# Optimization experiments

Hardware: AMD Instinct MI355X
Metric: run time of the kernel (lower is better)

Reference implementation:

```python
import jax, jax.numpy as jnp
import numpy as np

D = 512       # hidden_size (attention defaults hardcode 512)
N = 8         # num_heads
H = D // N    # depth per head = 64
FF = 2048     # FFN filter size (hardcoded)
EPS = 1e-6


def _layer_norm(x, gamma, beta):
    # matches functional layer_norm: biased variance, eps inside sqrt
    mean = jnp.mean(x, axis=-1, keepdims=True)
    var = jnp.mean((x - mean) ** 2, axis=-1, keepdims=True)
    return gamma * ((x - mean) / jnp.sqrt(var + EPS)) + beta


def setup_inputs() -> dict:
    key = jax.random.key(0)
    ks = jax.random.split(key, 12)
    B, S = 8, 1024
    s = lambda k, shape, scale: jax.random.normal(k, shape, jnp.float32) * scale
    return {
        "inputs": s(ks[0], (B, S, D), 1.0),
        "attention_bias": jnp.zeros((B, 1, 1, S), jnp.float32),
        "ln1_g": jnp.ones((D,), jnp.float32),
        "ln1_b": jnp.zeros((D,), jnp.float32),
        "wq": s(ks[1], (D, N, H), D ** -0.5),
        "wk": s(ks[2], (D, N, H), D ** -0.5),
        "wv": s(ks[3], (D, N, H), D ** -0.5),
        "wo": s(ks[4], (N, H, D), D ** -0.5),
        "ln2_g": jnp.ones((D,), jnp.float32),
        "ln2_b": jnp.zeros((D,), jnp.float32),
        "w1": s(ks[5], (D, FF), D ** -0.5),
        "b1": jnp.zeros((FF,), jnp.float32),
        "w2": s(ks[6], (FF, D), FF ** -0.5),
        "b2": jnp.zeros((D,), jnp.float32),
    }


def reference(inputs, attention_bias, ln1_g, ln1_b, wq, wk, wv, wo,
              ln2_g, ln2_b, w1, b1, w2, b2):
    # --- self-attention block (pre-LN, residual) ---
    y = _layer_norm(inputs, ln1_g, ln1_b)
    q = jnp.einsum('bsd,dnh->bsnh', y, wq) * (H ** -0.5)
    k = jnp.einsum('bsd,dnh->bsnh', y, wk)
    v = jnp.einsum('bsd,dnh->bsnh', y, wv)
    # logits[b,n,f,t] = sum_h k[b,t,n,h] * q[b,f,n,h]
    logits = jnp.einsum('btnh,bfnh->bnft', k, q) + attention_bias
    weights = jax.nn.softmax(logits, axis=3)
    attn = jnp.einsum('bnft,btnh->bfnh', weights, v)
    attn_out = jnp.einsum('bfnh,nhd->bfd', attn, wo)
    x = inputs + attn_out

    # --- FFN block (pre-LN, residual) ---
    y2 = _layer_norm(x, ln2_g, ln2_b)
    h = jax.nn.relu(jnp.einsum('bsd,df->bsf', y2, w1) + b1)
    ffn_out = jnp.einsum('bsf,fd->bsd', h, w2) + b2
    return x + ffn_out
```

## Files before the change

### kernel.cpp

```cpp
#include <hip/hip_runtime.h>
#include <stdint.h>

typedef unsigned short u16;
typedef __attribute__((ext_vector_type(8))) __bf16 bf16x8;
typedef __attribute__((ext_vector_type(2))) __bf16 bf16x2;
typedef __attribute__((ext_vector_type(4))) float f32x4;

__device__ __forceinline__ float bf2f(u16 u) {
    union { unsigned int i; float f; } c; c.i = ((unsigned int)u) << 16; return c.f;
}
__device__ __forceinline__ u16 f2bf_sw(float f) {
    union { float f; unsigned int i; } c; c.f = f;
    unsigned int u = c.i;
    u += 0x7FFFu + ((u >> 16) & 1u);
    return (u16)(u >> 16);
}
__device__ __forceinline__ unsigned f2bf2(float lo, float hi) {
#if __has_builtin(__builtin_amdgcn_cvt_pk_bf16_f32)
    union { bf16x2 v; unsigned u; } c;
    c.v = __builtin_amdgcn_cvt_pk_bf16_f32(lo, hi);
    return c.u;
#else
    return (unsigned)f2bf_sw(lo) | ((unsigned)f2bf_sw(hi) << 16);
#endif
}
__device__ __forceinline__ u16 f2bf(float f) {
#if __has_builtin(__builtin_amdgcn_cvt_pk_bf16_f32)
    return (u16)(f2bf2(f, 0.f) & 0xFFFFu);
#else
    return f2bf_sw(f);
#endif
}
__device__ __forceinline__ bool sniff_f32(const unsigned* probe) {
    return probe && ((*probe & 0xFFFFu) == 0u);
}
__device__ __forceinline__ float lde(const void* p, size_t i, bool isf32) {
    return isf32 ? ((const float*)p)[i] : bf2f(((const u16*)p)[i]);
}
__device__ __forceinline__ void g2lds16(const void* g, void* l) {
    __builtin_amdgcn_global_load_lds(
        (__attribute__((address_space(1))) void*)(uintptr_t)g,
        (__attribute__((address_space(3))) void*)(unsigned int)(uintptr_t)l,
        16, 0, 0);
}

__global__ void prep_weights(const void* __restrict__ wq, const void* __restrict__ wk,
                             const void* __restrict__ wv, const void* __restrict__ wo,
                             const void* __restrict__ w1, const void* __restrict__ w2,
                             u16* __restrict__ wqkvT, u16* __restrict__ woT,
                             u16* __restrict__ w1T, u16* __restrict__ w2T,
                             const unsigned* probe) {
    __shared__ u16 t[32][33];
    const bool isf32 = sniff_f32(probe);
    const int id = blockIdx.x;
    const void* src; u16* dst; int R, C, cb, rb; float scale = 1.f;
    if (id < 1024) {
        const int which = id >> 8, tl = id & 255;
        R = 512; C = 512; cb = (tl & 15) * 32; rb = (tl >> 4) * 32;
        if (which == 0)      { src = wq; dst = wqkvT;              scale = 0.18033688011112042f; }
        else if (which == 1) { src = wk; dst = wqkvT + 512 * 512; }
        else if (which == 2) { src = wv; dst = wqkvT + 1024 * 512; }
        else                 { src = wo; dst = woT; }
    } else if (id < 2048) {
        const int tl = id - 1024; src = w1; dst = w1T; R = 512; C = 2048;
        cb = (tl & 63) * 32; rb = (tl >> 6) * 32;
    } else {
        const int tl = id - 2048; src = w2; dst = w2T; R = 2048; C = 512;
        cb = (tl & 15) * 32; rb = (tl >> 4) * 32;
    }
    const int tx = threadIdx.x, ty = threadIdx.y;
#pragma unroll
    for (int i = 0; i < 4; i++)
        t[ty + i * 8][tx] = f2bf(lde(src, (size_t)(rb + ty + i * 8) * C + cb + tx, isf32));
    __syncthreads();
#pragma unroll
    for (int i = 0; i < 4; i++) {
        float v = bf2f(t[tx][ty + i * 8]) * scale;
        dst[(size_t)(cb + ty + i * 8) * R + rb + tx] = f2bf(v);
    }
}

__global__ __launch_bounds__(256) void ln_any(const void* __restrict__ x,
                                              const void* __restrict__ gw,
                                              const void* __restrict__ bw,
                                              u16* __restrict__ y,
                                              const unsigned* probe_x,
                                              const unsigned* probe_gb) {
    const bool xf32 = sniff_f32(probe_x);
    const bool gf32 = sniff_f32(probe_gb);
    const int lane = threadIdx.x & 63, wave = threadIdx.x >> 6;
    const int r = blockIdx.x * 4 + wave;
    union U8 { uint4 v; u16 s[8]; };
    float xs[8];
    if (xf32) {
        const float4* xr = (const float4*)((const float*)x + (size_t)r * 512 + lane * 8);
        float4 p0 = xr[0], p1 = xr[1];
        xs[0]=p0.x; xs[1]=p0.y; xs[2]=p0.z; xs[3]=p0.w;
        xs[4]=p1.x; xs[5]=p1.y; xs[6]=p1.z; xs[7]=p1.w;
    } else {
        U8 xu; xu.v = *(const uint4*)((const u16*)x + (size_t)r * 512 + lane * 8);
#pragma unroll
        for (int j = 0; j < 8; j++) xs[j] = bf2f(xu.s[j]);
    }
    float s1 = 0.f, s2 = 0.f;
#pragma unroll
    for (int j = 0; j < 8; j++) { s1 += xs[j]; s2 += xs[j] * xs[j]; }
#pragma unroll
    for (int d = 1; d < 64; d <<= 1) { s1 += __shfl_xor(s1, d); s2 += __shfl_xor(s2, d); }
    const float mean = s1 * (1.f / 512.f);
    const float var = s2 * (1.f / 512.f) - mean * mean;
    const float rstd = rsqrtf(var + 1e-6f);
    float gs[8], bs[8];
    if (gf32) {
        const float4* gr = (const float4*)((const float*)gw + lane * 8);
        const float4* br = (const float4*)((const float*)bw + lane * 8);
        float4 g0 = gr[0], g1 = gr[1], b0 = br[0], b1 = br[1];
        gs[0]=g0.x; gs[1]=g0.y; gs[2]=g0.z; gs[3]=g0.w; gs[4]=g1.x; gs[5]=g1.y; gs[6]=g1.z; gs[7]=g1.w;
        bs[0]=b0.x; bs[1]=b0.y; bs[2]=b0.z; bs[3]=b0.w; bs[4]=b1.x; bs[5]=b1.y; bs[6]=b1.z; bs[7]=b1.w;
    } else {
        U8 gu; gu.v = *(const uint4*)((const u16*)gw + lane * 8);
        U8 bu; bu.v = *(const uint4*)((const u16*)bw + lane * 8);
#pragma unroll
        for (int j = 0; j < 8; j++) { gs[j] = bf2f(gu.s[j]); bs[j] = bf2f(bu.s[j]); }
    }
    uint4 ov;
    float o[8];
#pragma unroll
    for (int j = 0; j < 8; j++) o[j] = gs[j] * ((xs[j] - mean) * rstd) + bs[j];
    ov.x = f2bf2(o[0], o[1]); ov.y = f2bf2(o[2], o[3]);
    ov.z = f2bf2(o[4], o[5]); ov.w = f2bf2(o[6], o[7]);
    *(uint4*)(y + (size_t)r * 512 + lane * 8) = ov;
}

template <int EPI, int TM>
__global__ __launch_bounds__(256, 2) void gemm_bt(const u16* __restrict__ A,
                                                  const u16* __restrict__ Bt,
                                                  const void* __restrict__ bias,
                                                  const void* __restrict__ res,
                                                  void* __restrict__ out,
                                                  u16* __restrict__ out2,
                                                  const unsigned* probe,
                                                  int M, int N, int K) {
    constexpr int ACH = TM / 16;
    constexpr int MI = TM / 32;
    __shared__ __align__(16) u16 lA[2][TM * 32];
    __shared__ __align__(16) u16 lB[2][128 * 32];
    const int tid = threadIdx.x, wave = tid >> 6, lane = tid & 63;
    const int m0 = blockIdx.x * TM, n0 = blockIdx.y * 128;
    const int wm = (wave >> 1) * (TM / 2), wn = (wave & 1) * 64;
    const int row = lane & 15, quad = lane >> 4;
    f32x4 acc[MI][4];
#pragma unroll
    for (int i = 0; i < MI; i++)
#pragma unroll
        for (int j = 0; j < 4; j++) acc[i][j] = (f32x4){0.f, 0.f, 0.f, 0.f};
    const u16* Ab = A + (size_t)m0 * K;
    const u16* Bb = Bt + (size_t)n0 * K;

    auto stage = [&](int buf, int k0) {
#pragma unroll
        for (int c = 0; c < (ACH + 8 + 3) / 4; c++) {
            const int ch = c * 4 + wave;
            if (ch < ACH) {
                const int e = ch * 64 + lane;
                const int r = e >> 2, col = (e & 3) * 8;
                g2lds16(Ab + (size_t)r * K + k0 + col, (char*)lA[buf] + ch * 1024);
            } else if (ch < ACH + 8) {
                const int c2 = ch - ACH;
                const int e = c2 * 64 + lane;
                const int r = e >> 2, col = (e & 3) * 8;
                g2lds16(Bb + (size_t)r * K + k0 + col, (char*)lB[buf] + c2 * 1024);
            }
        }
    };

    stage(0, 0);
    int cur = 0;
    for (int k0 = 0; k0 < K; k0 += 32) {
        __syncthreads();
        if (k0 + 32 < K) stage(cur ^ 1, k0 + 32);
        bf16x8 af[MI], bfr[4];
#pragma unroll
        for (int t = 0; t < MI; t++)
            af[t]  = *(const bf16x8*)(lA[cur] + (wm + t * 16 + row) * 32 + quad * 8);
#pragma unroll
        for (int t = 0; t < 4; t++)
            bfr[t] = *(const bf16x8*)(lB[cur] + (wn + t * 16 + row) * 32 + quad * 8);
#pragma unroll
        for (int i = 0; i < MI; i++)
#pragma unroll
            for (int j = 0; j < 4; j++)
                acc[i][j] = __builtin_amdgcn_mfma_f32_16x16x32_bf16(af[i], bfr[j], acc[i][j], 0, 0, 0);
        cur ^= 1;
    }
    const bool isf32 = sniff_f32(probe);
#pragma unroll
    for (int i = 0; i < MI; i++) {
        const int gm = m0 + wm + i * 16 + quad * 4;
#pragma unroll
        for (int j = 0; j < 4; j++) {
            const int gn = n0 + wn + j * 16 + row;
            float bv = 0.f;
            if (EPI == 2 || EPI == 3) bv = lde(bias, gn, isf32);
#pragma unroll
            for (int r = 0; r < 4; r++) {
                float v = acc[i][j][r];
                const int gmr = gm + r;
                size_t idx = (size_t)gmr * N + gn;
                if (EPI == 1) {
                    ((u16*)out)[idx] = f2bf(v + lde(res, idx, isf32));
                } else if (EPI == 2) {
                    v += bv;
                    ((u16*)out)[idx] = f2bf(v > 0.f ? v : 0.f);
                } else if (EPI == 3) {
                    v += bv + bf2f(((const u16*)res)[idx]);
                    if (isf32) ((float*)out)[idx] = v;
                    else       ((u16*)out)[idx] = f2bf(v);
                } else {
                    if (gn < 1024) {
                        ((u16*)out)[(size_t)gmr * 1024 + gn] = f2bf(v);
                    } else {
                        const int j2 = gn - 1024, n = j2 >> 6, h2 = j2 & 63;
                        const int b = gmr >> 10, t = gmr & 1023;
                        const int ut = t & 31, vt = ut & 15;
                        const int tP = (t & ~31) | ((vt >> 2) * 8 + ((ut >> 4) << 2) + (vt & 3));
                        out2[(((size_t)b * 8 + n) * 64 + h2) * 1024 + tP] = f2bf(v);
                    }
                }
            }
        }
    }
}

__global__ __launch_bounds__(256, 4) void attn_fused(const u16* __restrict__ qk,
                                                     const u16* __restrict__ vT,
                                                     const void* __restrict__ biasp,
                                                     u16* __restrict__ attn,
                                                     const unsigned* probe) {
    __shared__ __align__(16) u16 lQ[64 * 64];
    __shared__ __align__(16) u16 lK[128 * 64];
    __shared__ __align__(16) u16 lV[64 * 128];
    const bool isf32 = sniff_f32(probe);
    const int tid = threadIdx.x, wave = tid >> 6, lane = tid & 63;
    const int row = lane & 15, quad = lane >> 4;
    const int bn = blockIdx.x, b = bn >> 3, n = bn & 7;
    const int f0 = blockIdx.y * 64;
    const u16* Qg = qk + (size_t)(b * 1024 + f0) * 1024 + n * 64;
    const u16* Kg = qk + (size_t)(b * 1024) * 1024 + 512 + n * 64;
    const u16* Vg = vT + (size_t)bn * 65536;

#pragma unroll
    for (int j = 0; j < 2; j++) {
        const int ch = wave * 2 + j, e = ch * 64 + lane;
        const int rq = e >> 3, cq = ((e & 7) ^ (rq & 7)) * 8;
        g2lds16(Qg + (size_t)rq * 1024 + cq, (char*)lQ + ch * 1024);
    }
    __syncthreads();
    const int fr = wave * 16 + row;
    bf16x8 bq[2];
#pragma unroll
    for (int ks = 0; ks < 2; ks++)
        bq[ks] = *(const bf16x8*)(lQ + fr * 64 + (((ks * 4 + quad) ^ (fr & 7)) * 8));

    float l_i = 0.f;
    f32x4 oacc[4];
#pragma unroll
    for (int h = 0; h < 4; h++) oacc[h] = (f32x4){0.f, 0.f, 0.f, 0.f};

    for (int t0 = 0; t0 < 1024; t0 += 128) {
        __syncthreads();
#pragma unroll
        for (int j = 0; j < 4; j++) {
            const int ch = wave * 4 + j, e = ch * 64 + lane;
            const int rk = e >> 3, ck = ((e & 7) ^ (rk & 7)) * 8;
            g2lds16(Kg + (size_t)(t0 + rk) * 1024 + ck, (char*)lK + ch * 1024);
            const int rv = e >> 4, cv = ((e & 15) ^ (rv & 7)) * 8;
            g2lds16(Vg + (size_t)rv * 1024 + t0 + cv, (char*)lV + ch * 1024);
        }
        __syncthreads();
        f32x4 s[8];
#pragma unroll
        for (int nt = 0; nt < 8; nt++) s[nt] = (f32x4){0.f, 0.f, 0.f, 0.f};
#pragma unroll
        for (int nt = 0; nt < 8; nt++) {
            const int tr = nt * 16 + row;
#pragma unroll
            for (int ks = 0; ks < 2; ks++) {
                bf16x8 ak = *(const bf16x8*)(lK + tr * 64 + (((ks * 4 + quad) ^ (tr & 7)) * 8));
                s[nt] = __builtin_amdgcn_mfma_f32_16x16x32_bf16(ak, bq[ks], s[nt], 0, 0, 0);
            }
        }
#pragma unroll
        for (int nt = 0; nt < 8; nt++) {
            const size_t bidx = (size_t)b * 1024 + t0 + nt * 16 + quad * 4;
            float bv4[4];
            if (isf32) {
                float4 t4 = *(const float4*)((const float*)biasp + bidx);
                bv4[0] = t4.x; bv4[1] = t4.y; bv4[2] = t4.z; bv4[3] = t4.w;
            } else {
                union { uint2 v; u16 s[4]; } bu;
                bu.v = *(const uint2*)((const u16*)biasp + bidx);
#pragma unroll
                for (int r = 0; r < 4; r++) bv4[r] = bf2f(bu.s[r]);
            }
#pragma unroll
            for (int r = 0; r < 4; r++) {
                float p = __builtin_exp2f(fmaf(bv4[r], 1.4426950408889634f, s[nt][r]));
                s[nt][r] = p;
                l_i += p;
            }
        }
#pragma unroll
        for (int ks = 0; ks < 4; ks++) {
            union { unsigned u[4]; bf16x8 v8; } bb;
            bb.u[0] = f2bf2(s[ks * 2][0],     s[ks * 2][1]);
            bb.u[1] = f2bf2(s[ks * 2][2],     s[ks * 2][3]);
            bb.u[2] = f2bf2(s[ks * 2 + 1][0], s[ks * 2 + 1][1]);
            bb.u[3] = f2bf2(s[ks * 2 + 1][2], s[ks * 2 + 1][3]);
#pragma unroll
            for (int ht = 0; ht < 4; ht++) {
                const int vr = ht * 16 + row;
                bf16x8 av = *(const bf16x8*)(lV + vr * 128 + (((ks * 4 + quad) ^ (vr & 7)) * 8));
                oacc[ht] = __builtin_amdgcn_mfma_f32_16x16x32_bf16(av, bb.v8, oacc[ht], 0, 0, 0);
            }
        }
    }
    l_i += __shfl_xor(l_i, 16);
    l_i += __shfl_xor(l_i, 32);
    const float inv = 1.f / l_i;
    const int f = f0 + wave * 16 + row;
#pragma unroll
    for (int ht = 0; ht < 4; ht++) {
        uint2 ov;
        ov.x = f2bf2(oacc[ht][0] * inv, oacc[ht][1] * inv);
        ov.y = f2bf2(oacc[ht][2] * inv, oacc[ht][3] * inv);
        *(uint2*)(attn + (size_t)(b * 1024 + f) * 512 + n * 64 + ht * 16 + quad * 4) = ov;
    }
}

extern "C" void kernel_launch(void* const* d_in, const int* in_sizes, int n_in,
                              void* d_out, int out_size, void* d_ws, size_t ws_size,
                              hipStream_t stream) {
    const void* inp  = d_in[0];
    const void* ab   = d_in[1];
    const void* ln1g = d_in[2];
    const void* ln1b = d_in[3];
    const void* wq   = d_in[4];
    const void* wk   = d_in[5];
    const void* wv   = d_in[6];
    const void* wo   = d_in[7];
    const void* ln2g = d_in[8];
    const void* ln2b = d_in[9];
    const void* w1   = d_in[10];
    const void* b1   = d_in[11];
    const void* w2   = d_in[12];
    const void* b2   = d_in[13];
    const unsigned* probe = (const unsigned*)d_in[2];

    char* ws = (char*)d_ws;
    size_t off = 0;
    auto alloc = [&](size_t bytes) -> void* { void* p = ws + off; off += bytes; return p; };
    u16* wqkvT = (u16*)alloc(1536 * 512 * 2);
    u16* woT   = (u16*)alloc(512 * 512 * 2);
    u16* w1T   = (u16*)alloc(2048 * 512 * 2);
    u16* w2T   = (u16*)alloc(512 * 2048 * 2);
    u16* ybuf  = (u16*)alloc((size_t)8192 * 512 * 2);
    u16* qk    = (u16*)alloc((size_t)8192 * 1024 * 2);
    u16* vT    = (u16*)alloc((size_t)64 * 64 * 1024 * 2);
    u16* attn  = (u16*)alloc((size_t)8192 * 512 * 2);
    u16* xbf   = (u16*)alloc((size_t)8192 * 512 * 2);
    u16* hbuf  = qk;

    prep_weights<<<3072, dim3(32, 8), 0, stream>>>(wq, wk, wv, wo, w1, w2,
                                                   wqkvT, woT, w1T, w2T, probe);
    ln_any<<<2048, 256, 0, stream>>>(inp, ln1g, ln1b, ybuf, probe, probe);
    gemm_bt<4, 128><<<dim3(64, 12), 256, 0, stream>>>(ybuf, wqkvT, nullptr, nullptr, qk, vT, nullptr, 8192, 1536, 512);
    attn_fused<<<dim3(64, 16), 256, 0, stream>>>(qk, vT, ab, attn, probe);
    gemm_bt<1, 64><<<dim3(128, 4), 256, 0, stream>>>(attn, woT, nullptr, inp, xbf, nullptr, probe, 8192, 512, 512);
    ln_any<<<2048, 256, 0, stream>>>(xbf, ln2g, ln2b, ybuf, nullptr, probe);
    gemm_bt<2, 128><<<dim3(64, 16), 256, 0, stream>>>(ybuf, w1T, b1, nullptr, hbuf, nullptr, probe, 8192, 2048, 512);
    gemm_bt<3, 64><<<dim3(128, 4), 256, 0, stream>>>(hbuf, w2T, b2, xbf, (u16*)d_out, nullptr, probe, 8192, 512, 2048);
}
```

Baseline: 253.5 us.

## Double-buffer K/V tiles in attention kernel to overlap loads with MFMA

The attention kernel now splits each 128-key step into two 64-key tiles held in ping-pong LDS buffers. The loads for the next tile are issued before computing on the current one, so global-to-LDS traffic can overlap with the MFMA and softmax work. Bias loads are hoisted ahead of the QK MFMAs and the swizzle offset is precomputed once per thread. Total LDS use stays the same, but the loop depends on correct barrier placement and async load completion semantics of g2lds16.

```diff
diff --git a/kernel.cpp b/kernel.cpp
--- a/kernel.cpp
+++ b/kernel.cpp
@@ -238,11 +238,13 @@
                                                      u16* __restrict__ attn,
                                                      const unsigned* probe) {
     __shared__ __align__(16) u16 lQ[64 * 64];
-    __shared__ __align__(16) u16 lK[128 * 64];
-    __shared__ __align__(16) u16 lV[64 * 128];
+    __shared__ __align__(16) u16 lK[2][64 * 64];
+    __shared__ __align__(16) u16 lV[2][64 * 64];
     const bool isf32 = sniff_f32(probe);
     const int tid = threadIdx.x, wave = tid >> 6, lane = tid & 63;
     const int row = lane & 15, quad = lane >> 4;
+    const int r7 = row & 7;
+    const int g0 = (quad ^ r7) * 8;
     const int bn = blockIdx.x, b = bn >> 3, n = bn & 7;
     const int f0 = blockIdx.y * 64;
     const u16* Qg = qk + (size_t)(b * 1024 + f0) * 1024 + n * 64;
@@ -255,63 +257,73 @@
         const int rq = e >> 3, cq = ((e & 7) ^ (rq & 7)) * 8;
         g2lds16(Qg + (size_t)rq * 1024 + cq, (char*)lQ + ch * 1024);
     }
+
+    auto stage = [&](int buf, int t0) {
+#pragma unroll
+        for (int j = 0; j < 4; j++) {
+            const int ch = wave * 4 + j;
+            if (ch < 8) {
+                const int e = ch * 64 + lane;
+                const int rk = e >> 3, ck = ((e & 7) ^ (rk & 7)) * 8;
+                g2lds16(Kg + (size_t)(t0 + rk) * 1024 + ck, (char*)&lK[buf][0] + ch * 1024);
+            } else {
+                const int e = (ch - 8) * 64 + lane;
+                const int rv = e >> 3, cv = ((e & 7) ^ (rv & 7)) * 8;
+                g2lds16(Vg + (size_t)rv * 1024 + t0 + cv, (char*)&lV[buf][0] + (ch - 8) * 1024);
+            }
+        }
+    };
+
+    stage(0, 0);
     __syncthreads();
+
     const int fr = wave * 16 + row;
     bf16x8 bq[2];
 #pragma unroll
     for (int ks = 0; ks < 2; ks++)
-        bq[ks] = *(const bf16x8*)(lQ + fr * 64 + (((ks * 4 + quad) ^ (fr & 7)) * 8));
+        bq[ks] = *(const bf16x8*)(lQ + fr * 64 + (g0 ^ (ks * 32)));
 
     float l_i = 0.f;
     f32x4 oacc[4];
 #pragma unroll
     for (int h = 0; h < 4; h++) oacc[h] = (f32x4){0.f, 0.f, 0.f, 0.f};
 
-    for (int t0 = 0; t0 < 1024; t0 += 128) {
-        __syncthreads();
-#pragma unroll
-        for (int j = 0; j < 4; j++) {
-            const int ch = wave * 4 + j, e = ch * 64 + lane;
-            const int rk = e >> 3, ck = ((e & 7) ^ (rk & 7)) * 8;
-            g2lds16(Kg + (size_t)(t0 + rk) * 1024 + ck, (char*)lK + ch * 1024);
-            const int rv = e >> 4, cv = ((e & 15) ^ (rv & 7)) * 8;
-            g2lds16(Vg + (size_t)rv * 1024 + t0 + cv, (char*)lV + ch * 1024);
-        }
-        __syncthreads();
-        f32x4 s[8];
-#pragma unroll
-        for (int nt = 0; nt < 8; nt++) s[nt] = (f32x4){0.f, 0.f, 0.f, 0.f};
-#pragma unroll
-        for (int nt = 0; nt < 8; nt++) {
-            const int tr = nt * 16 + row;
-#pragma unroll
-            for (int ks = 0; ks < 2; ks++) {
-                bf16x8 ak = *(const bf16x8*)(lK + tr * 64 + (((ks * 4 + quad) ^ (tr & 7)) * 8));
-                s[nt] = __builtin_amdgcn_mfma_f32_16x16x32_bf16(ak, bq[ks], s[nt], 0, 0, 0);
-            }
-        }
-#pragma unroll
-        for (int nt = 0; nt < 8; nt++) {
+    auto compute = [&](int buf, int t0) {
+        float bv4[4][4];
+#pragma unroll
+        for (int nt = 0; nt < 4; nt++) {
             const size_t bidx = (size_t)b * 1024 + t0 + nt * 16 + quad * 4;
-            float bv4[4];
             if (isf32) {
                 float4 t4 = *(const float4*)((const float*)biasp + bidx);
-                bv4[0] = t4.x; bv4[1] = t4.y; bv4[2] = t4.z; bv4[3] = t4.w;
+                bv4[nt][0] = t4.x; bv4[nt][1] = t4.y; bv4[nt][2] = t4.z; bv4[nt][3] = t4.w;
             } else {
                 union { uint2 v; u16 s[4]; } bu;
                 bu.v = *(const uint2*)((const u16*)biasp + bidx);
 #pragma unroll
-                for (int r = 0; r < 4; r++) bv4[r] = bf2f(bu.s[r]);
-            }
+                for (int r = 0; r < 4; r++) bv4[nt][r] = bf2f(bu.s[r]);
+            }
+        }
+        f32x4 s[4];
+#pragma unroll
+        for (int nt = 0; nt < 4; nt++) s[nt] = (f32x4){0.f, 0.f, 0.f, 0.f};
+#pragma unroll
+        for (int nt = 0; nt < 4; nt++) {
+#pragma unroll
+            for (int ks = 0; ks < 2; ks++) {
+                bf16x8 ak = *(const bf16x8*)(&lK[buf][0] + (nt * 16 + row) * 64 + (g0 ^ (ks * 32)));
+                s[nt] = __builtin_amdgcn_mfma_f32_16x16x32_bf16(ak, bq[ks], s[nt], 0, 0, 0);
+            }
+        }
+#pragma unroll
+        for (int nt = 0; nt < 4; nt++)
 #pragma unroll
             for (int r = 0; r < 4; r++) {
-                float p = __builtin_exp2f(fmaf(bv4[r], 1.4426950408889634f, s[nt][r]));
+                float p = __builtin_exp2f(fmaf(bv4[nt][r], 1.4426950408889634f, s[nt][r]));
                 s[nt][r] = p;
                 l_i += p;
             }
-        }
-#pragma unroll
-        for (int ks = 0; ks < 4; ks++) {
+#pragma unroll
+        for (int ks = 0; ks < 2; ks++) {
             union { unsigned u[4]; bf16x8 v8; } bb;
             bb.u[0] = f2bf2(s[ks * 2][0],     s[ks * 2][1]);
             bb.u[1] = f2bf2(s[ks * 2][2],     s[ks * 2][3]);
@@ -319,12 +331,21 @@
             bb.u[3] = f2bf2(s[ks * 2 + 1][2], s[ks * 2 + 1][3]);
 #pragma unroll
             for (int ht = 0; ht < 4; ht++) {
-                const int vr = ht * 16 + row;
-                bf16x8 av = *(const bf16x8*)(lV + vr * 128 + (((ks * 4 + quad) ^ (vr & 7)) * 8));
+                bf16x8 av = *(const bf16x8*)(&lV[buf][0] + (ht * 16 + row) * 64 + (g0 ^ (ks * 32)));
                 oacc[ht] = __builtin_amdgcn_mfma_f32_16x16x32_bf16(av, bb.v8, oacc[ht], 0, 0, 0);
             }
         }
-    }
+    };
+
+    for (int t0 = 0; t0 < 1024; t0 += 128) {
+        __syncthreads();
+        stage(1, t0 + 64);
+        compute(0, t0);
+        __syncthreads();
+        if (t0 + 128 < 1024) stage(0, t0 + 128);
+        compute(1, t0 + 64);
+    }
+
     l_i += __shfl_xor(l_i, 16);
     l_i += __shfl_xor(l_i, 32);
     const float inv = 1.f / l_i;
```

Result: no change. 251.3 us (-0.9%).

## Split attention keys across waves with per-wave double-buffered KV and LDS reduction

Applied to the files above, without the earlier changes.

Restructures the fused attention kernel so each of the four waves handles all 64 query rows over its own quarter of the key range (split-K). Each wave stages its K/V tiles into a private double buffer with explicit vmcnt waits, so no block-wide barriers are needed inside the loop. The bias is preloaded into LDS. Partial outputs and row sums are then reduced through LDS at the end. The cost is 76KB of shared memory and many more accumulator registers, with the occupancy hint dropped, so fewer blocks fit per CU.

```diff
diff --git a/kernel.cpp b/kernel.cpp
--- a/kernel.cpp
+++ b/kernel.cpp
@@ -232,16 +232,18 @@
     }
 }
 
-__global__ __launch_bounds__(256, 4) void attn_fused(const u16* __restrict__ qk,
-                                                     const u16* __restrict__ vT,
-                                                     const void* __restrict__ biasp,
-                                                     u16* __restrict__ attn,
-                                                     const unsigned* probe) {
-    __shared__ __align__(16) u16 lQ[64 * 64];
-    __shared__ __align__(16) u16 lK[128 * 64];
-    __shared__ __align__(16) u16 lV[64 * 128];
+__global__ __launch_bounds__(256) void attn_fused(const u16* __restrict__ qk,
+                                                  const u16* __restrict__ vT,
+                                                  const void* __restrict__ biasp,
+                                                  u16* __restrict__ attn,
+                                                  const unsigned* probe) {
+    __shared__ __align__(16) char smem[76 * 1024];
+    u16*  lQ  = (u16*)smem;
+    char* kvb = smem + 8192;
+    char* lBb = smem + 8192 + 65536;
+
     const bool isf32 = sniff_f32(probe);
-    const int tid = threadIdx.x, wave = tid >> 6, lane = tid & 63;
+    const int tid = threadIdx.x, w = tid >> 6, lane = tid & 63;
     const int row = lane & 15, quad = lane >> 4;
     const int bn = blockIdx.x, b = bn >> 3, n = bn & 7;
     const int f0 = blockIdx.y * 64;
@@ -249,92 +251,158 @@
     const u16* Kg = qk + (size_t)(b * 1024) * 1024 + 512 + n * 64;
     const u16* Vg = vT + (size_t)bn * 65536;
 
+    u16* lKw = (u16*)(kvb + w * 16384);
+    u16* lVw = (u16*)(kvb + w * 16384 + 8192);
+    char* lBw = lBb + w * 1024;
+    const int tb = w * 256;
+
 #pragma unroll
     for (int j = 0; j < 2; j++) {
-        const int ch = wave * 2 + j, e = ch * 64 + lane;
+        const int ch = w * 2 + j, e = ch * 64 + lane;
         const int rq = e >> 3, cq = ((e & 7) ^ (rq & 7)) * 8;
         g2lds16(Qg + (size_t)rq * 1024 + cq, (char*)lQ + ch * 1024);
     }
+    if (isf32) {
+        g2lds16((const float*)biasp + (size_t)b * 1024 + tb + lane * 4, lBw);
+    } else if (lane < 32) {
+        g2lds16((const u16*)biasp + (size_t)b * 1024 + tb + lane * 8, lBw);
+    }
+    auto stageKV = [&](int buf, int t0) {
+#pragma unroll
+        for (int c = 0; c < 4; c++) {
+            const int rk = c * 8 + (lane >> 3);
+            const int ck = ((lane & 7) ^ (rk & 7)) * 8;
+            g2lds16(Kg + (size_t)(t0 + rk) * 1024 + ck, (char*)lKw + buf * 4096 + c * 1024);
+            const int rv = c * 16 + (lane >> 2);
+            const int cv = ((lane & 3) ^ (rv & 3)) * 8;
+            g2lds16(Vg + (size_t)rv * 1024 + t0 + cv, (char*)lVw + buf * 4096 + c * 1024);
+        }
+    };
+    stageKV(0, tb);
     __syncthreads();
-    const int fr = wave * 16 + row;
-    bf16x8 bq[2];
-#pragma unroll
-    for (int ks = 0; ks < 2; ks++)
-        bq[ks] = *(const bf16x8*)(lQ + fr * 64 + (((ks * 4 + quad) ^ (fr & 7)) * 8));
-
-    float l_i = 0.f;
-    f32x4 oacc[4];
-#pragma unroll
-    for (int h = 0; h < 4; h++) oacc[h] = (f32x4){0.f, 0.f, 0.f, 0.f};
-
-    for (int t0 = 0; t0 < 1024; t0 += 128) {
-        __syncthreads();
-#pragma unroll
-        for (int j = 0; j < 4; j++) {
-            const int ch = wave * 4 + j, e = ch * 64 + lane;
-            const int rk = e >> 3, ck = ((e & 7) ^ (rk & 7)) * 8;
-            g2lds16(Kg + (size_t)(t0 + rk) * 1024 + ck, (char*)lK + ch * 1024);
-            const int rv = e >> 4, cv = ((e & 15) ^ (rv & 7)) * 8;
-            g2lds16(Vg + (size_t)rv * 1024 + t0 + cv, (char*)lV + ch * 1024);
-        }
-        __syncthreads();
-        f32x4 s[8];
-#pragma unroll
-        for (int nt = 0; nt < 8; nt++) s[nt] = (f32x4){0.f, 0.f, 0.f, 0.f};
-#pragma unroll
-        for (int nt = 0; nt < 8; nt++) {
-            const int tr = nt * 16 + row;
-#pragma unroll
-            for (int ks = 0; ks < 2; ks++) {
-                bf16x8 ak = *(const bf16x8*)(lK + tr * 64 + (((ks * 4 + quad) ^ (tr & 7)) * 8));
-                s[nt] = __builtin_amdgcn_mfma_f32_16x16x32_bf16(ak, bq[ks], s[nt], 0, 0, 0);
-            }
-        }
-#pragma unroll
-        for (int nt = 0; nt < 8; nt++) {
-            const size_t bidx = (size_t)b * 1024 + t0 + nt * 16 + quad * 4;
+
+    const int gK0 = (quad ^ (row & 7)) * 8;
+    const int gK1 = ((4 + quad) ^ (row & 7)) * 8;
+    const int gV  = (quad ^ (row & 3)) * 8;
+    bf16x8 bq[4][2];
+#pragma unroll
+    for (int fb = 0; fb < 4; fb++) {
+        bq[fb][0] = *(const bf16x8*)(lQ + (fb * 16 + row) * 64 + gK0);
+        bq[fb][1] = *(const bf16x8*)(lQ + (fb * 16 + row) * 64 + gK1);
+    }
+
+    float l4[4] = {0.f, 0.f, 0.f, 0.f};
+    f32x4 oacc[4][4];
+#pragma unroll
+    for (int i = 0; i < 4; i++)
+#pragma unroll
+        for (int j = 0; j < 4; j++) oacc[i][j] = (f32x4){0.f, 0.f, 0.f, 0.f};
+
+    auto compute = [&](int buf, int ti) {
+        const u16* lKc = lKw + buf * 2048;
+        const u16* lVc = lVw + buf * 2048;
+        f32x4 s[2][4];
+#pragma unroll
+        for (int tn = 0; tn < 2; tn++)
+#pragma unroll
+            for (int fb = 0; fb < 4; fb++) s[tn][fb] = (f32x4){0.f, 0.f, 0.f, 0.f};
+#pragma unroll
+        for (int tn = 0; tn < 2; tn++) {
+            bf16x8 ak0 = *(const bf16x8*)(lKc + (tn * 16 + row) * 64 + gK0);
+#pragma unroll
+            for (int fb = 0; fb < 4; fb++)
+                s[tn][fb] = __builtin_amdgcn_mfma_f32_16x16x32_bf16(ak0, bq[fb][0], s[tn][fb], 0, 0, 0);
+            bf16x8 ak1 = *(const bf16x8*)(lKc + (tn * 16 + row) * 64 + gK1);
+#pragma unroll
+            for (int fb = 0; fb < 4; fb++)
+                s[tn][fb] = __builtin_amdgcn_mfma_f32_16x16x32_bf16(ak1, bq[fb][1], s[tn][fb], 0, 0, 0);
+        }
+#pragma unroll
+        for (int tn = 0; tn < 2; tn++) {
+            const int tl = ti * 32 + tn * 16 + quad * 4;
             float bv4[4];
             if (isf32) {
-                float4 t4 = *(const float4*)((const float*)biasp + bidx);
+                float4 t4 = *(const float4*)((const float*)lBw + tl);
                 bv4[0] = t4.x; bv4[1] = t4.y; bv4[2] = t4.z; bv4[3] = t4.w;
             } else {
                 union { uint2 v; u16 s[4]; } bu;
-                bu.v = *(const uint2*)((const u16*)biasp + bidx);
+                bu.v = *(const uint2*)((const u16*)lBw + tl);
 #pragma unroll
                 for (int r = 0; r < 4; r++) bv4[r] = bf2f(bu.s[r]);
             }
 #pragma unroll
-            for (int r = 0; r < 4; r++) {
-                float p = __builtin_exp2f(fmaf(bv4[r], 1.4426950408889634f, s[nt][r]));
-                s[nt][r] = p;
-                l_i += p;
-            }
-        }
-#pragma unroll
-        for (int ks = 0; ks < 4; ks++) {
-            union { unsigned u[4]; bf16x8 v8; } bb;
-            bb.u[0] = f2bf2(s[ks * 2][0],     s[ks * 2][1]);
-            bb.u[1] = f2bf2(s[ks * 2][2],     s[ks * 2][3]);
-            bb.u[2] = f2bf2(s[ks * 2 + 1][0], s[ks * 2 + 1][1]);
-            bb.u[3] = f2bf2(s[ks * 2 + 1][2], s[ks * 2 + 1][3]);
-#pragma unroll
-            for (int ht = 0; ht < 4; ht++) {
-                const int vr = ht * 16 + row;
-                bf16x8 av = *(const bf16x8*)(lV + vr * 128 + (((ks * 4 + quad) ^ (vr & 7)) * 8));
-                oacc[ht] = __builtin_amdgcn_mfma_f32_16x16x32_bf16(av, bb.v8, oacc[ht], 0, 0, 0);
-            }
-        }
-    }
-    l_i += __shfl_xor(l_i, 16);
-    l_i += __shfl_xor(l_i, 32);
-    const float inv = 1.f / l_i;
-    const int f = f0 + wave * 16 + row;
-#pragma unroll
-    for (int ht = 0; ht < 4; ht++) {
-        uint2 ov;
-        ov.x = f2bf2(oacc[ht][0] * inv, oacc[ht][1] * inv);
-        ov.y = f2bf2(oacc[ht][2] * inv, oacc[ht][3] * inv);
-        *(uint2*)(attn + (size_t)(b * 1024 + f) * 512 + n * 64 + ht * 16 + quad * 4) = ov;
+            for (int fb = 0; fb < 4; fb++)
+#pragma unroll
+                for (int r = 0; r < 4; r++) {
+                    float p = __builtin_exp2f(fmaf(bv4[r], 1.4426950408889634f, s[tn][fb][r]));
+                    s[tn][fb][r] = p;
+                    l4[fb] += p;
+                }
+        }
+        union { unsigned u[4]; bf16x8 v8; } bb[4];
+#pragma unroll
+        for (int fb = 0; fb < 4; fb++) {
+            bb[fb].u[0] = f2bf2(s[0][fb][0], s[0][fb][1]);
+            bb[fb].u[1] = f2bf2(s[0][fb][2], s[0][fb][3]);
+            bb[fb].u[2] = f2bf2(s[1][fb][0], s[1][fb][1]);
+            bb[fb].u[3] = f2bf2(s[1][fb][2], s[1][fb][3]);
+        }
+#pragma unroll
+        for (int ht = 0; ht < 4; ht++) {
+            bf16x8 av = *(const bf16x8*)(lVc + (ht * 16 + row) * 32 + gV);
+#pragma unroll
+            for (int fb = 0; fb < 4; fb++)
+                oacc[ht][fb] = __builtin_amdgcn_mfma_f32_16x16x32_bf16(av, bb[fb].v8, oacc[ht][fb], 0, 0, 0);
+        }
+    };
+
+    int cur = 0;
+#pragma unroll 1
+    for (int ti = 0; ti < 7; ti++) {
+        stageKV(cur ^ 1, tb + (ti + 1) * 32);
+        asm volatile("s_waitcnt vmcnt(8)" ::: "memory");
+        compute(cur, ti);
+        cur ^= 1;
+    }
+    asm volatile("s_waitcnt vmcnt(0)" ::: "memory");
+    compute(cur, 7);
+
+    float* lL = (float*)lQ;
+#pragma unroll
+    for (int fb = 0; fb < 4; fb++) {
+        l4[fb] += __shfl_xor(l4[fb], 16);
+        l4[fb] += __shfl_xor(l4[fb], 32);
+    }
+    if (quad == 0) {
+#pragma unroll
+        for (int fb = 0; fb < 4; fb++) lL[w * 64 + fb * 16 + row] = l4[fb];
+    }
+    {
+        float* Fw = (float*)(kvb + w * 16384);
+        const int hs = (quad ^ (row & 3)) * 4;
+#pragma unroll
+        for (int ht = 0; ht < 4; ht++)
+#pragma unroll
+            for (int fb = 0; fb < 4; fb++)
+                *(f32x4*)(Fw + (fb * 16 + row) * 64 + ht * 16 + hs) = oacc[ht][fb];
+    }
+    __syncthreads();
+    {
+        const int fl = w * 16 + row;
+        const int hs = (quad ^ (row & 3)) * 4;
+        float lf = lL[fl] + lL[64 + fl] + lL[128 + fl] + lL[192 + fl];
+        const float inv = 1.f / lf;
+#pragma unroll
+        for (int ht = 0; ht < 4; ht++) {
+            f32x4 o = (f32x4){0.f, 0.f, 0.f, 0.f};
+#pragma unroll
+            for (int v = 0; v < 4; v++)
+                o += *(const f32x4*)((const float*)(kvb + v * 16384) + fl * 64 + ht * 16 + hs);
+            uint2 ov;
+            ov.x = f2bf2(o[0] * inv, o[1] * inv);
+            ov.y = f2bf2(o[2] * inv, o[3] * inv);
+            *(uint2*)(attn + (size_t)(b * 1024 + f0 + fl) * 512 + n * 64 + ht * 16 + quad * 4) = ov;
+        }
     }
 }
 
```

Result: no change. 255.5 us (+0.8%).

## Double query tile per attention block to reuse staged K/V tiles

Applied to the files above, without the earlier changes.

Each attention block now handles 128 query rows instead of 64, with every wave owning two 16-row query fragments that share each K and V fragment loaded from LDS. This halves the grid and the total global-to-LDS K/V staging traffic, and reuses each LDS read for two MFMAs. The Q load and the first K/V stage are merged behind a single barrier. In exchange, register use roughly doubles for the accumulators and launch bounds drop to 2 blocks per SM, so there are only 512 blocks and latency hiding may be weaker.

```diff
diff --git a/kernel.cpp b/kernel.cpp
--- a/kernel.cpp
+++ b/kernel.cpp
@@ -232,43 +232,31 @@
     }
 }
 
-__global__ __launch_bounds__(256, 4) void attn_fused(const u16* __restrict__ qk,
+__global__ __launch_bounds__(256, 2) void attn_fused(const u16* __restrict__ qk,
                                                      const u16* __restrict__ vT,
                                                      const void* __restrict__ biasp,
                                                      u16* __restrict__ attn,
                                                      const unsigned* probe) {
-    __shared__ __align__(16) u16 lQ[64 * 64];
+    __shared__ __align__(16) u16 lQ[128 * 64];
     __shared__ __align__(16) u16 lK[128 * 64];
     __shared__ __align__(16) u16 lV[64 * 128];
     const bool isf32 = sniff_f32(probe);
     const int tid = threadIdx.x, wave = tid >> 6, lane = tid & 63;
     const int row = lane & 15, quad = lane >> 4;
+    const int g0 = (quad ^ (row & 7)) * 8;
     const int bn = blockIdx.x, b = bn >> 3, n = bn & 7;
-    const int f0 = blockIdx.y * 64;
+    const int f0 = blockIdx.y * 128;
     const u16* Qg = qk + (size_t)(b * 1024 + f0) * 1024 + n * 64;
     const u16* Kg = qk + (size_t)(b * 1024) * 1024 + 512 + n * 64;
     const u16* Vg = vT + (size_t)bn * 65536;
 
 #pragma unroll
-    for (int j = 0; j < 2; j++) {
-        const int ch = wave * 2 + j, e = ch * 64 + lane;
+    for (int j = 0; j < 4; j++) {
+        const int ch = wave * 4 + j, e = ch * 64 + lane;
         const int rq = e >> 3, cq = ((e & 7) ^ (rq & 7)) * 8;
         g2lds16(Qg + (size_t)rq * 1024 + cq, (char*)lQ + ch * 1024);
     }
-    __syncthreads();
-    const int fr = wave * 16 + row;
-    bf16x8 bq[2];
-#pragma unroll
-    for (int ks = 0; ks < 2; ks++)
-        bq[ks] = *(const bf16x8*)(lQ + fr * 64 + (((ks * 4 + quad) ^ (fr & 7)) * 8));
-
-    float l_i = 0.f;
-    f32x4 oacc[4];
-#pragma unroll
-    for (int h = 0; h < 4; h++) oacc[h] = (f32x4){0.f, 0.f, 0.f, 0.f};
-
-    for (int t0 = 0; t0 < 1024; t0 += 128) {
-        __syncthreads();
+    auto stageKV = [&](int t0) {
 #pragma unroll
         for (int j = 0; j < 4; j++) {
             const int ch = wave * 4 + j, e = ch * 64 + lane;
@@ -277,18 +265,40 @@
             const int rv = e >> 4, cv = ((e & 15) ^ (rv & 7)) * 8;
             g2lds16(Vg + (size_t)rv * 1024 + t0 + cv, (char*)lV + ch * 1024);
         }
-        __syncthreads();
-        f32x4 s[8];
-#pragma unroll
-        for (int nt = 0; nt < 8; nt++) s[nt] = (f32x4){0.f, 0.f, 0.f, 0.f};
+    };
+    stageKV(0);
+    __syncthreads();
+
+    bf16x8 bq[2][2];
+#pragma unroll
+    for (int h = 0; h < 2; h++) {
+        const int fr = h * 64 + wave * 16 + row;
+        bq[h][0] = *(const bf16x8*)(lQ + fr * 64 + g0);
+        bq[h][1] = *(const bf16x8*)(lQ + fr * 64 + (g0 ^ 32));
+    }
+
+    float l4[2] = {0.f, 0.f};
+    f32x4 oacc[2][4];
+#pragma unroll
+    for (int i = 0; i < 2; i++)
+#pragma unroll
+        for (int j = 0; j < 4; j++) oacc[i][j] = (f32x4){0.f, 0.f, 0.f, 0.f};
+
+    auto compute = [&](int t0) {
+        f32x4 s[2][8];
+#pragma unroll
+        for (int h = 0; h < 2; h++)
+#pragma unroll
+            for (int nt = 0; nt < 8; nt++) s[h][nt] = (f32x4){0.f, 0.f, 0.f, 0.f};
 #pragma unroll
         for (int nt = 0; nt < 8; nt++) {
             const int tr = nt * 16 + row;
-#pragma unroll
-            for (int ks = 0; ks < 2; ks++) {
-                bf16x8 ak = *(const bf16x8*)(lK + tr * 64 + (((ks * 4 + quad) ^ (tr & 7)) * 8));
-                s[nt] = __builtin_amdgcn_mfma_f32_16x16x32_bf16(ak, bq[ks], s[nt], 0, 0, 0);
-            }
+            bf16x8 ak0 = *(const bf16x8*)(lK + tr * 64 + g0);
+            s[0][nt] = __builtin_amdgcn_mfma_f32_16x16x32_bf16(ak0, bq[0][0], s[0][nt], 0, 0, 0);
+            s[1][nt] = __builtin_amdgcn_mfma_f32_16x16x32_bf16(ak0, bq[1][0], s[1][nt], 0, 0, 0);
+            bf16x8 ak1 = *(const bf16x8*)(lK + tr * 64 + (g0 ^ 32));
+            s[0][nt] = __builtin_amdgcn_mfma_f32_16x16x32_bf16(ak1, bq[0][1], s[0][nt], 0, 0, 0);
+            s[1][nt] = __builtin_amdgcn_mfma_f32_16x16x32_bf16(ak1, bq[1][1], s[1][nt], 0, 0, 0);
         }
 #pragma unroll
         for (int nt = 0; nt < 8; nt++) {
@@ -304,37 +314,55 @@
                 for (int r = 0; r < 4; r++) bv4[r] = bf2f(bu.s[r]);
             }
 #pragma unroll
-            for (int r = 0; r < 4; r++) {
-                float p = __builtin_exp2f(fmaf(bv4[r], 1.4426950408889634f, s[nt][r]));
-                s[nt][r] = p;
-                l_i += p;
+            for (int h = 0; h < 2; h++)
+#pragma unroll
+                for (int r = 0; r < 4; r++) {
+                    float p = __builtin_exp2f(fmaf(bv4[r], 1.4426950408889634f, s[h][nt][r]));
+                    s[h][nt][r] = p;
+                    l4[h] += p;
+                }
+        }
+#pragma unroll
+        for (int ks = 0; ks < 4; ks++) {
+            union { unsigned u[4]; bf16x8 v8; } bb[2];
+#pragma unroll
+            for (int h = 0; h < 2; h++) {
+                bb[h].u[0] = f2bf2(s[h][ks * 2][0],     s[h][ks * 2][1]);
+                bb[h].u[1] = f2bf2(s[h][ks * 2][2],     s[h][ks * 2][3]);
+                bb[h].u[2] = f2bf2(s[h][ks * 2 + 1][0], s[h][ks * 2 + 1][1]);
+                bb[h].u[3] = f2bf2(s[h][ks * 2 + 1][2], s[h][ks * 2 + 1][3]);
             }
-        }
-#pragma unroll
-        for (int ks = 0; ks < 4; ks++) {
-            union { unsigned u[4]; bf16x8 v8; } bb;
-            bb.u[0] = f2bf2(s[ks * 2][0],     s[ks * 2][1]);
-            bb.u[1] = f2bf2(s[ks * 2][2],     s[ks * 2][3]);
-            bb.u[2] = f2bf2(s[ks * 2 + 1][0], s[ks * 2 + 1][1]);
-            bb.u[3] = f2bf2(s[ks * 2 + 1][2], s[ks * 2 + 1][3]);
 #pragma unroll
             for (int ht = 0; ht < 4; ht++) {
                 const int vr = ht * 16 + row;
-                bf16x8 av = *(const bf16x8*)(lV + vr * 128 + (((ks * 4 + quad) ^ (vr & 7)) * 8));
-                oacc[ht] = __builtin_amdgcn_mfma_f32_16x16x32_bf16(av, bb.v8, oacc[ht], 0, 0, 0);
+                bf16x8 av = *(const bf16x8*)(lV + vr * 128 + (g0 ^ (ks * 32)));
+                oacc[0][ht] = __builtin_amdgcn_mfma_f32_16x16x32_bf16(av, bb[0].v8, oacc[0][ht], 0, 0, 0);
+                oacc[1][ht] = __builtin_amdgcn_mfma_f32_16x16x32_bf16(av, bb[1].v8, oacc[1][ht], 0, 0, 0);
             }
         }
-    }
-    l_i += __shfl_xor(l_i, 16);
-    l_i += __shfl_xor(l_i, 32);
-    const float inv = 1.f / l_i;
-    const int f = f0 + wave * 16 + row;
-#pragma unroll
-    for (int ht = 0; ht < 4; ht++) {
-        uint2 ov;
-        ov.x = f2bf2(oacc[ht][0] * inv, oacc[ht][1] * inv);
-        ov.y = f2bf2(oacc[ht][2] * inv, oacc[ht][3] * inv);
-        *(uint2*)(attn + (size_t)(b * 1024 + f) * 512 + n * 64 + ht * 16 + quad * 4) = ov;
+    };
+
+    compute(0);
+    for (int t0 = 128; t0 < 1024; t0 += 128) {
+        __syncthreads();
+        stageKV(t0);
+        __syncthreads();
+        compute(t0);
+    }
+
+#pragma unroll
+    for (int h = 0; h < 2; h++) {
+        l4[h] += __shfl_xor(l4[h], 16);
+        l4[h] += __shfl_xor(l4[h], 32);
+        const float inv = 1.f / l4[h];
+        const int f = f0 + h * 64 + wave * 16 + row;
+#pragma unroll
+        for (int ht = 0; ht < 4; ht++) {
+            uint2 ov;
+            ov.x = f2bf2(oacc[h][ht][0] * inv, oacc[h][ht][1] * inv);
+            ov.y = f2bf2(oacc[h][ht][2] * inv, oacc[h][ht][3] * inv);
+            *(uint2*)(attn + (size_t)(b * 1024 + f) * 512 + n * 64 + ht * 16 + quad * 4) = ov;
+        }
     }
 }
 
@@ -375,7 +403,7 @@
                                                    wqkvT, woT, w1T, w2T, probe);
     ln_any<<<2048, 256, 0, stream>>>(inp, ln1g, ln1b, ybuf, probe, probe);
     gemm_bt<4, 128><<<dim3(64, 12), 256, 0, stream>>>(ybuf, wqkvT, nullptr, nullptr, qk, vT, nullptr, 8192, 1536, 512);
-    attn_fused<<<dim3(64, 16), 256, 0, stream>>>(qk, vT, ab, attn, probe);
+    attn_fused<<<dim3(64, 8), 256, 0, stream>>>(qk, vT, ab, attn, probe);
     gemm_bt<1, 64><<<dim3(128, 4), 256, 0, stream>>>(attn, woT, nullptr, inp, xbf, nullptr, probe, 8192, 512, 512);
     ln_any<<<2048, 256, 0, stream>>>(xbf, ln2g, ln2b, ybuf, nullptr, probe);
     gemm_bt<2, 128><<<dim3(64, 16), 256, 0, stream>>>(ybuf, w1T, b1, nullptr, hbuf, nullptr, probe, 8192, 2048, 512);
```

After: 253.3 us. No clear change (-0.1%).
